# Optimization experiments

Measured on AMD Instinct MI355X. Metric: run time of the kernel, lower is better.

## Reference

```python
import jax, jax.numpy as jnp
import numpy as np

INPUT_SIZE = 1024
OUTPUT_SIZE = 1024
B, S = 4, 2048


def setup_inputs() -> dict:
    key = jax.random.key(0)
    k1, k2, k3, k4, k5, k6 = jax.random.split(key, 6)
    scale = 1.0 / np.sqrt(INPUT_SIZE)
    return {
        "inputs_for_keys": jax.random.normal(k1, (B, S, INPUT_SIZE), jnp.float32),
        "inputs_for_values": jax.random.normal(k2, (B, S, INPUT_SIZE), jnp.float32),
        "inputs_for_queries": jax.random.normal(k3, (B, S, INPUT_SIZE), jnp.float32),
        "W_k": jax.random.normal(k4, (INPUT_SIZE, OUTPUT_SIZE), jnp.float32) * scale,
        "W_v": jax.random.normal(k5, (INPUT_SIZE, OUTPUT_SIZE), jnp.float32) * scale,
        "W_q": jax.random.normal(k6, (INPUT_SIZE, OUTPUT_SIZE), jnp.float32) * scale,
    }


def reference(inputs_for_keys, inputs_for_values, inputs_for_queries, W_k, W_v, W_q):
    # Linear projections (bias=False): x @ W  -> [B, S, D_out]
    K = jnp.einsum("bsi,io->bso", inputs_for_keys, W_k)
    V = jnp.einsum("bsi,io->bso", inputs_for_values, W_v)
    Q = jnp.einsum("bqi,io->bqo", inputs_for_queries, W_q)
    d_k = K.shape[-1]
    # scores: [B, Sq, Sk], scaled by sqrt(embedding_size of K)
    scores = jnp.einsum("bqd,bkd->bqk", Q, K) / jnp.sqrt(jnp.asarray(d_k, Q.dtype))
    # causal mask: positions k > q masked to -inf (use_mask=True since is_self_attention)
    q_idx = jnp.arange(Q.shape[1])[:, None]
    k_idx = jnp.arange(K.shape[1])[None, :]
    scores = jnp.where(k_idx > q_idx, jnp.asarray(-jnp.inf, scores.dtype), scores)
    weights = jax.nn.softmax(scores, axis=-1)
    # output: [B, Sq, D_out]
    return jnp.einsum("bqk,bkd->bqd", weights, V)
```

## Files before the change

### kernel.cpp

```cpp
#include <hip/hip_runtime.h>


typedef __attribute__((ext_vector_type(8))) short short8;
typedef __attribute__((ext_vector_type(4))) float floatx4;

static constexpr long long XE = 8388608LL;
static constexpr long long WE = 1048576LL;

static __device__ __forceinline__ unsigned short f2b(float f) {
  unsigned u = __builtin_bit_cast(unsigned, f);
  u = (u + 0x7fffu + ((u >> 16) & 1u)) >> 16;
  return (unsigned short)u;
}

static __device__ __forceinline__ void gload16(const unsigned short* g, unsigned short* l) {
  __builtin_amdgcn_global_load_lds(
      (const __attribute__((address_space(1))) unsigned int*)g,
      (__attribute__((address_space(3))) unsigned int*)l, 16, 0, 0);
}

#define VMCNT(n) asm volatile("s_waitcnt vmcnt(" #n ")" ::: "memory")
#define LGKM0() asm volatile("s_waitcnt lgkmcnt(0)" ::: "memory")
#define BARRIER() do { asm volatile("" ::: "memory"); __builtin_amdgcn_s_barrier(); asm volatile("" ::: "memory"); } while (0)

#define STAGE(base, matoff, h, slot, kt) do {                                  \
    const unsigned short* _s = (base) + (h) * 131072 + (kt) * 64;              \
    char* _d = sb + (slot) * 65536 + (matoff) + (h) * 16384 + dwave;           \
    gload16(_s, (unsigned short*)_d);                                          \
    gload16(_s + 65536, (unsigned short*)(_d + 8192));                         \
  } while (0)

#define READ_A(slot, mb) do {                                                  \
    const char* _p = sb + (slot) * 65536 + aoffb + (mb) * 2048;                \
    af[0][0] = *(const short8*)(_p + c0);        af[0][1] = *(const short8*)(_p + c1); \
    af[1][0] = *(const short8*)(_p + 2048 + c0); af[1][1] = *(const short8*)(_p + 2048 + c1); \
    af[2][0] = *(const short8*)(_p + 4096 + c0); af[2][1] = *(const short8*)(_p + 4096 + c1); \
    af[3][0] = *(const short8*)(_p + 6144 + c0); af[3][1] = *(const short8*)(_p + 6144 + c1); \
  } while (0)

#define READ_B(slot, nb, bfx) do {                                             \
    const char* _p = sb + (slot) * 65536 + boffb + (nb) * 2048;                \
    bfx[0][0] = *(const short8*)(_p + c0);        bfx[0][1] = *(const short8*)(_p + c1); \
    bfx[1][0] = *(const short8*)(_p + 2048 + c0); bfx[1][1] = *(const short8*)(_p + 2048 + c1); \
  } while (0)

#define MF16(MB, NB, bfx) do {                                                 \
    __builtin_amdgcn_s_setprio(1);                                             \
    _Pragma("unroll")                                                          \
    for (int _m = 0; _m < 4; ++_m) {                                           \
      _Pragma("unroll")                                                        \
      for (int _n = 0; _n < 2; ++_n) {                                         \
        acc[(MB) + _m][(NB) + _n] = __builtin_amdgcn_mfma_f32_16x16x32_bf16(   \
            af[_m][0], bfx[_n][0], acc[(MB) + _m][(NB) + _n], 0, 0, 0);        \
        acc[(MB) + _m][(NB) + _n] = __builtin_amdgcn_mfma_f32_16x16x32_bf16(   \
            af[_m][1], bfx[_n][1], acc[(MB) + _m][(NB) + _n], 0, 0, 0);        \
      } }                                                                      \
    __builtin_amdgcn_s_setprio(0);                                             \
  } while (0)

#define KLOOP8()                                                               \
  STAGE(Ab, 0, 0, 0, 0);     STAGE(Ab, 0, 1, 0, 0);                            \
  STAGE(Bb, 32768, 0, 0, 0); STAGE(Bb, 32768, 1, 0, 0);                        \
  STAGE(Bb, 32768, 0, 1, 1); STAGE(Bb, 32768, 1, 1, 1);                        \
  VMCNT(4);                                                                    \
  BARRIER();                                                                   \
  for (int t = 0; t < 8; ++t) {                                                \
    const int kt1 = 2 * t + 1, kt2 = 2 * t + 2, kt3 = 2 * t + 3;               \
    const bool pf = t < 7;                                                     \
    READ_A(0, 0); READ_B(0, 0, bf0);                                           \
    STAGE(Ab, 0, 0, 1, kt1);                                                   \
    BARRIER(); LGKM0();                                                        \
    MF16(0, 0, bf0);                                                           \
    BARRIER();                                                                 \
    READ_B(0, 2, bf1);                                                         \
    STAGE(Ab, 0, 1, 1, kt1);                                                   \
    BARRIER(); LGKM0();                                                        \
    MF16(0, 2, bf1);                                                           \
    BARRIER();                                                                 \
    READ_A(0, 4);                                                              \
    if (pf) STAGE(Bb, 32768, 0, 0, kt2);                                       \
    BARRIER(); LGKM0();                                                        \
    MF16(4, 2, bf1);                                                           \
    BARRIER();                                                                 \
    if (pf) STAGE(Bb, 32768, 1, 0, kt2);                                       \
    BARRIER();                                                                 \
    MF16(4, 0, bf0);                                                           \
    if (pf) { VMCNT(4); } else { VMCNT(0); }                                   \
    BARRIER();                                                                 \
    READ_A(1, 0); READ_B(1, 0, bf0);                                           \
    if (pf) STAGE(Ab, 0, 0, 0, kt2);                                           \
    BARRIER(); LGKM0();                                                        \
    MF16(0, 0, bf0);                                                           \
    BARRIER();                                                                 \
    READ_B(1, 2, bf1);                                                         \
    if (pf) STAGE(Ab, 0, 1, 0, kt2);                                           \
    BARRIER(); LGKM0();                                                        \
    MF16(0, 2, bf1);                                                           \
    BARRIER();                                                                 \
    READ_A(1, 4);                                                              \
    if (pf) STAGE(Bb, 32768, 0, 1, kt3);                                       \
    BARRIER(); LGKM0();                                                        \
    MF16(4, 2, bf1);                                                           \
    BARRIER();                                                                 \
    if (pf) STAGE(Bb, 32768, 1, 1, kt3);                                       \
    BARRIER();                                                                 \
    MF16(4, 0, bf0);                                                           \
    if (pf) { VMCNT(4); } else { VMCNT(0); }                                   \
    BARRIER();                                                                 \
  }

__global__ __launch_bounds__(512, 2) void projTV8(
    const unsigned short* __restrict__ Xb, const unsigned short* __restrict__ WvT,
    const unsigned short* __restrict__ Gt, unsigned short* __restrict__ Tb,
    unsigned short* __restrict__ Vt) {
  extern __shared__ char sb[];
  const int orig = blockIdx.x;
  const int w = (orig & 7) * 32 + (orig >> 3);
  const unsigned short *Aop, *Bop;
  unsigned short* C;
  int ldc, bi, bj;
  if (w < 128) { Aop = Xb + XE; Bop = Gt; C = Tb; ldc = 1024; bi = w >> 2; bj = w & 3; }
  else { const int j = w - 128; Aop = WvT; Bop = Xb; C = Vt; ldc = 8192; bi = j & 3; bj = j >> 2; }

  const int tid = threadIdx.x, wave = tid >> 6, lane = tid & 63;
  const int wm = wave >> 2, wn = wave & 3, frow = lane & 15, hi = lane >> 4;
  const int r0 = tid >> 3, p0 = ((tid & 7) ^ (r0 & 7)) * 8;
  const int dwave = wave * 1024;
  const int sx = frow & 7;
  const int c0 = (hi ^ sx) * 16, c1 = ((4 + hi) ^ sx) * 16;
  const int aoffb = (wm * 128 + frow) * 128;
  const int boffb = 32768 + (wn * 64 + frow) * 128;
  const unsigned short* Ab = Aop + (long long)(bi * 256 + r0) * 1024 + p0;
  const unsigned short* Bb = Bop + (long long)(bj * 256 + r0) * 1024 + p0;

  short8 af[4][2], bf0[2][2], bf1[2][2];
  floatx4 acc[8][4] = {};

  KLOOP8();

  const long long crow0 = (long long)bi * 256 + wm * 128 + hi * 4;
  const int ccol = bj * 256 + wn * 64 + frow;
#pragma unroll
  for (int m = 0; m < 8; ++m)
#pragma unroll
    for (int j = 0; j < 4; ++j) {
      unsigned short* cp = C + (crow0 + m * 16 + j) * (long long)ldc + ccol;
#pragma unroll
      for (int n = 0; n < 4; ++n) cp[n * 16] = f2b(acc[m][n][j]);
    }
}

__global__ __launch_bounds__(512, 2) void scores_exp8(
    const unsigned short* __restrict__ Tb, const unsigned short* __restrict__ Xk,
    unsigned short* __restrict__ P, float* __restrict__ Rpart) {
  extern __shared__ char sb[];
  const int orig = blockIdx.x;
  const int w = (orig & 7) * 18 + (orig >> 3);
  const int b = w / 36;
  int t2 = w - b * 36;
  int bi = 0;
  while (t2 >= bi + 1) { t2 -= bi + 1; ++bi; }
  const int bj = t2;

  const unsigned short* Aop = Tb + (long long)b * 2048 * 1024;
  const unsigned short* Bop = Xk + (long long)b * 2048 * 1024;

  const int tid = threadIdx.x, wave = tid >> 6, lane = tid & 63;
  const int wm = wave >> 2, wn = wave & 3, frow = lane & 15, hi = lane >> 4;
  const int r0 = tid >> 3, p0 = ((tid & 7) ^ (r0 & 7)) * 8;
  const int dwave = wave * 1024;
  const int sx = frow & 7;
  const int c0 = (hi ^ sx) * 16, c1 = ((4 + hi) ^ sx) * 16;
  const int aoffb = (wm * 128 + frow) * 128;
  const int boffb = 32768 + (wn * 64 + frow) * 128;
  const unsigned short* Ab = Aop + (long long)(bi * 256 + r0) * 1024 + p0;
  const unsigned short* Bb = Bop + (long long)(bj * 256 + r0) * 1024 + p0;

  short8 af[4][2], bf0[2][2], bf1[2][2];
  floatx4 acc[8][4] = {};

  KLOOP8();

  const bool diag = (bi == bj);
  unsigned short* C = P + (long long)b * 2048 * 2048;
  float rs[8][4];
#pragma unroll
  for (int m = 0; m < 8; ++m)
#pragma unroll
    for (int j = 0; j < 4; ++j) {
      const int row_loc = wm * 128 + hi * 4 + m * 16 + j;
      const int row_glob = bi * 256 + row_loc;
      unsigned short* cp = C + (long long)row_glob * 2048 + bj * 256 + wn * 64 + frow;
      float s = 0.f;
#pragma unroll
      for (int n = 0; n < 4; ++n) {
        const int col = bj * 256 + wn * 64 + n * 16 + frow;
        float e = __expf(acc[m][n][j] * 0.03125f);
        if (diag && col > row_glob) e = 0.f;
        cp[n * 16] = f2b(e);
        s += e;
      }
      s += __shfl_xor(s, 1);
      s += __shfl_xor(s, 2);
      s += __shfl_xor(s, 4);
      s += __shfl_xor(s, 8);
      rs[m][j] = s;
    }
  __syncthreads();
  float* red = (float*)sb;
  if (frow == 0) {
#pragma unroll
    for (int m = 0; m < 8; ++m)
#pragma unroll
      for (int j = 0; j < 4; ++j)
        red[(wm * 128 + hi * 4 + m * 16 + j) * 4 + wn] = rs[m][j];
  }
  __syncthreads();
  if (tid < 256)
    Rpart[((long long)b * 8 + bj) * 2048 + bi * 256 + tid] =
        red[tid * 4] + red[tid * 4 + 1] + red[tid * 4 + 2] + red[tid * 4 + 3];
}

template <int NF>
static __device__ __forceinline__ void gemm_loop(
    const unsigned short* __restrict__ A, const unsigned short* __restrict__ Bt,
    int lda, int ldb, int nk, int bi, int bj,
    unsigned short* lA, unsigned short* lB, floatx4 acc[4][NF]) {
  const int t = threadIdx.x, wave = t >> 6, lane = t & 63;
  const int wr = wave >> 1, wc = wave & 1;
  const int sr = lane >> 3;
  const int sc = ((lane & 7) ^ sr) * 8;
  const unsigned short* gA = A + (long long)(bi * 128 + wave * 32 + sr) * lda + sc;
  const unsigned short* gB = Bt + (long long)(bj * (NF * 32) + wave * (NF * 8) + sr) * ldb + sc;
  unsigned short* lAw = lA + wave * 2048;
  unsigned short* lBw = lB + wave * (NF * 512);
  const int frow = lane & 15, hi = lane >> 4;

  for (int ks = 0; ks < nk; ++ks) {
    const long long k0 = (long long)ks * 64;
    __syncthreads();
#pragma unroll
    for (int g = 0; g < 4; ++g)
      gload16(gA + (long long)g * 8 * lda + k0, lAw + g * 512);
#pragma unroll
    for (int g = 0; g < NF; ++g)
      gload16(gB + (long long)g * 8 * ldb + k0, lBw + g * 512);
    __syncthreads();
#pragma unroll
    for (int kk = 0; kk < 2; ++kk) {
      const int ch = (kk * 4 + hi) ^ (frow & 7);
      short8 af[4], bf[NF];
#pragma unroll
      for (int m = 0; m < 4; ++m)
        af[m] = *(const short8*)&lA[(wr * 64 + m * 16 + frow) * 64 + ch * 8];
#pragma unroll
      for (int n = 0; n < NF; ++n)
        bf[n] = *(const short8*)&lB[(wc * (NF * 16) + n * 16 + frow) * 64 + ch * 8];
#pragma unroll
      for (int m = 0; m < 4; ++m)
#pragma unroll
        for (int n = 0; n < NF; ++n)
          acc[m][n] = __builtin_amdgcn_mfma_f32_16x16x32_bf16(af[m], bf[n], acc[m][n], 0, 0, 0);
    }
  }
}

__global__ __launch_bounds__(256) void gt_kernel(
    const unsigned short* __restrict__ WkB, const unsigned short* __restrict__ WqB,
    unsigned short* __restrict__ Gt) {
  __shared__ __align__(16) unsigned short lA[8192], lB[8192];
  floatx4 acc[4][4] = {};
  gemm_loop<4>(WkB, WqB, 1024, 1024, 16, blockIdx.x, blockIdx.y, lA, lB, acc);
  const int tid = threadIdx.x, wave = tid >> 6, lane = tid & 63;
  const int wr = wave >> 1, wc = wave & 1, frow = lane & 15, hi = lane >> 4;
  const long long crow0 = (long long)blockIdx.x * 128 + wr * 64 + hi * 4;
  const int ccol = blockIdx.y * 128 + wc * 64 + frow;
#pragma unroll
  for (int m = 0; m < 4; ++m)
#pragma unroll
    for (int j = 0; j < 4; ++j) {
      unsigned short* cp = Gt + (crow0 + m * 16 + j) * 1024 + ccol;
#pragma unroll
      for (int n = 0; n < 4; ++n) cp[n * 16] = f2b(acc[m][n][j]);
    }
}

__global__ __launch_bounds__(256) void rowsum(
    const float* __restrict__ Rpart, float* __restrict__ Rinv) {
  const int t = blockIdx.x * 256 + threadIdx.x;
  const int b = t >> 11, row = t & 2047;
  const int nb = (row >> 8) + 1;
  float s = 0.f;
  for (int bj = 0; bj < nb; ++bj) s += Rpart[(b * 8 + bj) * 2048 + row];
  Rinv[t] = 1.f / s;
}

__global__ __launch_bounds__(256) void pv_kernel(
    const unsigned short* __restrict__ P, const unsigned short* __restrict__ Vt,
    const float* __restrict__ Rinv, float* __restrict__ out) {
  __shared__ __align__(16) unsigned short lA[8192], lB[4096];
  const int orig = blockIdx.x;
  const int c = orig & 7, i = orig >> 3;
  const int bi = 15 - (i >> 3);
  const int rr = (i & 7) + c * 8;
  const int b = rr >> 4, bj = rr & 15;
  floatx4 acc[4][2] = {};
  gemm_loop<2>(P + (long long)b * 2048 * 2048, Vt + (long long)b * 2048, 2048, 8192,
               (bi + 1) * 2, bi, bj, lA, lB, acc);
  const int tid = threadIdx.x, wave = tid >> 6, lane = tid & 63;
  const int wr = wave >> 1, wc = wave & 1, frow = lane & 15, hi = lane >> 4;
  float* C = out + (long long)b * 2048 * 1024;
  const float* Ri = Rinv + b * 2048;
#pragma unroll
  for (int m = 0; m < 4; ++m)
#pragma unroll
    for (int j = 0; j < 4; ++j) {
      const int row = bi * 128 + wr * 64 + hi * 4 + m * 16 + j;
      const float riv = Ri[row];
      float* cp = C + (long long)row * 1024 + bj * 64 + wc * 32 + frow;
      cp[0] = acc[m][0][j] * riv;
      cp[16] = acc[m][1][j] * riv;
    }
}

__global__ __launch_bounds__(256) void cvtAll(
    const float* __restrict__ Xk, const float* __restrict__ Xv,
    const float* __restrict__ Xq, const float* __restrict__ Wq,
    const float* __restrict__ Wk, const float* __restrict__ Wv,
    unsigned short* __restrict__ Xb, unsigned short* __restrict__ WqB,
    unsigned short* __restrict__ WkB, unsigned short* __restrict__ WvT) {
  __shared__ unsigned short tile[64][65];
  const int bx = blockIdx.x, t = threadIdx.x;
  if (bx < 1536) {
    const int y = bx / 512, sub = bx - y * 512;
    const float* in = y == 0 ? Xv : (y == 1 ? Xq : Xk);
    unsigned short* o = Xb + (long long)y * XE;
    const int n8 = (int)(XE / 8), stride = 512 * 256;
    for (int i = sub * 256 + t; i < n8; i += stride) {
      float4 a = ((const float4*)in)[2 * i];
      float4 d = ((const float4*)in)[2 * i + 1];
      short8 v;
      v[0] = (short)f2b(a.x); v[1] = (short)f2b(a.y);
      v[2] = (short)f2b(a.z); v[3] = (short)f2b(a.w);
      v[4] = (short)f2b(d.x); v[5] = (short)f2b(d.y);
      v[6] = (short)f2b(d.z); v[7] = (short)f2b(d.w);
      ((short8*)o)[i] = v;
    }
  } else if (bx < 1792) {
    const int w2 = bx - 1536;
    const int y = w2 >> 7, sub = w2 & 127;
    const float* in = y == 0 ? Wq : Wk;
    unsigned short* o = y == 0 ? WqB : WkB;
    const int n8 = (int)(WE / 8), stride = 128 * 256;
    for (int i = sub * 256 + t; i < n8; i += stride) {
      float4 a = ((const float4*)in)[2 * i];
      float4 d = ((const float4*)in)[2 * i + 1];
      short8 v;
      v[0] = (short)f2b(a.x); v[1] = (short)f2b(a.y);
      v[2] = (short)f2b(a.z); v[3] = (short)f2b(a.w);
      v[4] = (short)f2b(d.x); v[5] = (short)f2b(d.y);
      v[6] = (short)f2b(d.z); v[7] = (short)f2b(d.w);
      ((short8*)o)[i] = v;
    }
  } else {
    const int v = bx - 1792;
    const int i0 = (v & 15) * 64, j0 = (v >> 4) * 64;
#pragma unroll
    for (int r = 0; r < 16; ++r) {
      int lin = r * 256 + t;
      int i = lin >> 6, j = lin & 63;
      tile[i][j] = f2b(Wv[(long long)(i0 + i) * 1024 + j0 + j]);
    }
    __syncthreads();
#pragma unroll
    for (int r = 0; r < 16; ++r) {
      int lin = r * 256 + t;
      int o = lin >> 6, i = lin & 63;
      WvT[(long long)(j0 + o) * 1024 + i0 + i] = tile[i][o];
    }
  }
}

extern "C" void kernel_launch(void* const* d_in, const int* in_sizes, int n_in,
                              void* d_out, int out_size, void* d_ws, size_t ws_size,
                              hipStream_t stream) {
  const float* Xk = (const float*)d_in[0];
  const float* Xv = (const float*)d_in[1];
  const float* Xq = (const float*)d_in[2];
  const float* Wk = (const float*)d_in[3];
  const float* Wv = (const float*)d_in[4];
  const float* Wq = (const float*)d_in[5];
  float* out = (float*)d_out;

  unsigned short* ws = (unsigned short*)d_ws;
  unsigned short* Xb = ws;
  unsigned short* WqB = ws + 3 * XE;
  unsigned short* WkB = WqB + WE;
  unsigned short* WvT = WkB + WE;
  unsigned short* Gt = WvT + WE;
  unsigned short* Tb = Gt + WE;
  unsigned short* Vt = Tb + XE;
  float* Rpart = (float*)(Vt + XE);
  float* Rinv = Rpart + 4 * 8 * 2048;
  unsigned short* Pbuf = ws;

  cvtAll<<<2048, 256, 0, stream>>>(Xk, Xv, Xq, Wq, Wk, Wv, Xb, WqB, WkB, WvT);
  gt_kernel<<<dim3(8, 8), 256, 0, stream>>>(WkB, WqB, Gt);
  projTV8<<<256, 512, 131072, stream>>>(Xb, WvT, Gt, Tb, Vt);
  scores_exp8<<<144, 512, 131072, stream>>>(Tb, Xb + 2 * XE, Pbuf, Rpart);
  rowsum<<<32, 256, 0, stream>>>(Rpart, Rinv);
  pv_kernel<<<1024, 256, 0, stream>>>(Pbuf, Vt, Rinv, out);
}
```

Before: 150.1 us.

## Fuse Xq fp32-to-bf16 conversion into projection GEMM A-operand loading

The Xq conversion pass is dropped from cvtAll. The T-projection GEMM now loads fp32 Xq directly into registers, converts it to bf16 and writes it into LDS inside the pipelined K loop, while the B operand still uses async global-to-LDS loads. This removes a 32MB fp32 read plus a 16MB bf16 write-and-reread round trip. In exchange the fp32 register staging adds register pressure, and launch bounds drop from 2 to 1 blocks per CU, which may reduce occupancy and latency hiding for both branches of the kernel.

```diff
diff --git a/kernel.cpp b/kernel.cpp
--- a/kernel.cpp
+++ b/kernel.cpp
@@ -109,19 +109,90 @@
     BARRIER();                                                                 \
   }
 
-__global__ __launch_bounds__(512, 2) void projTV8(
-    const unsigned short* __restrict__ Xb, const unsigned short* __restrict__ WvT,
-    const unsigned short* __restrict__ Gt, unsigned short* __restrict__ Tb,
-    unsigned short* __restrict__ Vt) {
+#define FLOAD(st, h, kt) do {                                                  \
+    const float* _s = Fq + (h) * 131072 + (kt) * 64;                           \
+    fr[st][0] = *(const floatx4*)_s;                                           \
+    fr[st][1] = *(const floatx4*)(_s + 4);                                     \
+    fr[st][2] = *(const floatx4*)(_s + 65536);                                 \
+    fr[st][3] = *(const floatx4*)(_s + 65540);                                 \
+  } while (0)
+
+#define FWRITE(st, h, slot) do {                                               \
+    char* _d = sb + (slot) * 65536 + (h) * 16384 + dwave + lane * 16;          \
+    short8 _v0, _v1;                                                           \
+    _Pragma("unroll")                                                          \
+    for (int _e = 0; _e < 4; ++_e) {                                           \
+      _v0[_e]     = (short)f2b(fr[st][0][_e]);                                 \
+      _v0[_e + 4] = (short)f2b(fr[st][1][_e]);                                 \
+      _v1[_e]     = (short)f2b(fr[st][2][_e]);                                 \
+      _v1[_e + 4] = (short)f2b(fr[st][3][_e]);                                 \
+    }                                                                          \
+    *(short8*)_d = _v0;                                                        \
+    *(short8*)(_d + 8192) = _v1;                                               \
+  } while (0)
+
+#define KLOOP8F()                                                              \
+  FLOAD(0, 0, 0); FLOAD(1, 1, 0);                                              \
+  STAGE(Bb, 32768, 0, 0, 0); STAGE(Bb, 32768, 1, 0, 0);                        \
+  STAGE(Bb, 32768, 0, 1, 1); STAGE(Bb, 32768, 1, 1, 1);                        \
+  FWRITE(0, 0, 0); FWRITE(1, 1, 0);                                            \
+  VMCNT(4); LGKM0();                                                           \
+  BARRIER();                                                                   \
+  for (int t = 0; t < 8; ++t) {                                                \
+    const int kt1 = 2 * t + 1, kt2 = 2 * t + 2, kt3 = 2 * t + 3;               \
+    const bool pf = t < 7;                                                     \
+    READ_A(0, 0); READ_B(0, 0, bf0);                                           \
+    FLOAD(0, 0, kt1);                                                          \
+    BARRIER(); LGKM0();                                                        \
+    MF16(0, 0, bf0);                                                           \
+    BARRIER();                                                                 \
+    READ_B(0, 2, bf1);                                                         \
+    FLOAD(1, 1, kt1);                                                          \
+    BARRIER(); LGKM0();                                                        \
+    MF16(0, 2, bf1);                                                           \
+    BARRIER();                                                                 \
+    READ_A(0, 4);                                                              \
+    if (pf) STAGE(Bb, 32768, 0, 0, kt2);                                       \
+    BARRIER(); LGKM0();                                                        \
+    MF16(4, 2, bf1);                                                           \
+    BARRIER();                                                                 \
+    if (pf) STAGE(Bb, 32768, 1, 0, kt2);                                       \
+    BARRIER();                                                                 \
+    MF16(4, 0, bf0);                                                           \
+    FWRITE(0, 0, 1); FWRITE(1, 1, 1);                                          \
+    if (pf) { VMCNT(4); } else { VMCNT(0); }                                   \
+    LGKM0();                                                                   \
+    BARRIER();                                                                 \
+    READ_A(1, 0); READ_B(1, 0, bf0);                                           \
+    if (pf) FLOAD(0, 0, kt2);                                                  \
+    BARRIER(); LGKM0();                                                        \
+    MF16(0, 0, bf0);                                                           \
+    BARRIER();                                                                 \
+    READ_B(1, 2, bf1);                                                         \
+    if (pf) FLOAD(1, 1, kt2);                                                  \
+    BARRIER(); LGKM0();                                                        \
+    MF16(0, 2, bf1);                                                           \
+    BARRIER();                                                                 \
+    READ_A(1, 4);                                                              \
+    if (pf) STAGE(Bb, 32768, 0, 1, kt3);                                       \
+    BARRIER(); LGKM0();                                                        \
+    MF16(4, 2, bf1);                                                           \
+    BARRIER();                                                                 \
+    if (pf) STAGE(Bb, 32768, 1, 1, kt3);                                       \
+    BARRIER();                                                                 \
+    MF16(4, 0, bf0);                                                           \
+    if (pf) { FWRITE(0, 0, 0); FWRITE(1, 1, 0); VMCNT(4); LGKM0(); }           \
+    else { VMCNT(0); }                                                         \
+    BARRIER();                                                                 \
+  }
+
+__global__ __launch_bounds__(512, 1) void projTV8(
+    const float* __restrict__ XqF, const unsigned short* __restrict__ Xb,
+    const unsigned short* __restrict__ WvT, const unsigned short* __restrict__ Gt,
+    unsigned short* __restrict__ Tb, unsigned short* __restrict__ Vt) {
   extern __shared__ char sb[];
   const int orig = blockIdx.x;
   const int w = (orig & 7) * 32 + (orig >> 3);
-  const unsigned short *Aop, *Bop;
-  unsigned short* C;
-  int ldc, bi, bj;
-  if (w < 128) { Aop = Xb + XE; Bop = Gt; C = Tb; ldc = 1024; bi = w >> 2; bj = w & 3; }
-  else { const int j = w - 128; Aop = WvT; Bop = Xb; C = Vt; ldc = 8192; bi = j & 3; bj = j >> 2; }
-
   const int tid = threadIdx.x, wave = tid >> 6, lane = tid & 63;
   const int wm = wave >> 2, wn = wave & 3, frow = lane & 15, hi = lane >> 4;
   const int r0 = tid >> 3, p0 = ((tid & 7) ^ (r0 & 7)) * 8;
@@ -130,13 +201,25 @@
   const int c0 = (hi ^ sx) * 16, c1 = ((4 + hi) ^ sx) * 16;
   const int aoffb = (wm * 128 + frow) * 128;
   const int boffb = 32768 + (wn * 64 + frow) * 128;
-  const unsigned short* Ab = Aop + (long long)(bi * 256 + r0) * 1024 + p0;
-  const unsigned short* Bb = Bop + (long long)(bj * 256 + r0) * 1024 + p0;
 
   short8 af[4][2], bf0[2][2], bf1[2][2];
+  floatx4 fr[2][4];
   floatx4 acc[8][4] = {};
-
-  KLOOP8();
+  unsigned short* C;
+  int ldc, bi, bj;
+
+  if (w < 128) {
+    bi = w >> 2; bj = w & 3; C = Tb; ldc = 1024;
+    const float* Fq = XqF + (long long)(bi * 256 + r0) * 1024 + p0;
+    const unsigned short* Bb = Gt + (long long)(bj * 256 + r0) * 1024 + p0;
+    KLOOP8F();
+  } else {
+    const int j = w - 128;
+    bi = j & 3; bj = j >> 2; C = Vt; ldc = 8192;
+    const unsigned short* Ab = WvT + (long long)(bi * 256 + r0) * 1024 + p0;
+    const unsigned short* Bb = Xb + (long long)(bj * 256 + r0) * 1024 + p0;
+    KLOOP8();
+  }
 
   const long long crow0 = (long long)bi * 256 + wm * 128 + hi * 4;
   const int ccol = bj * 256 + wn * 64 + frow;
@@ -325,16 +408,16 @@
 
 __global__ __launch_bounds__(256) void cvtAll(
     const float* __restrict__ Xk, const float* __restrict__ Xv,
-    const float* __restrict__ Xq, const float* __restrict__ Wq,
-    const float* __restrict__ Wk, const float* __restrict__ Wv,
-    unsigned short* __restrict__ Xb, unsigned short* __restrict__ WqB,
-    unsigned short* __restrict__ WkB, unsigned short* __restrict__ WvT) {
+    const float* __restrict__ Wq, const float* __restrict__ Wk,
+    const float* __restrict__ Wv, unsigned short* __restrict__ Xb,
+    unsigned short* __restrict__ WqB, unsigned short* __restrict__ WkB,
+    unsigned short* __restrict__ WvT) {
   __shared__ unsigned short tile[64][65];
   const int bx = blockIdx.x, t = threadIdx.x;
-  if (bx < 1536) {
-    const int y = bx / 512, sub = bx - y * 512;
-    const float* in = y == 0 ? Xv : (y == 1 ? Xq : Xk);
-    unsigned short* o = Xb + (long long)y * XE;
+  if (bx < 1024) {
+    const int y = bx >> 9, sub = bx & 511;
+    const float* in = y == 0 ? Xv : Xk;
+    unsigned short* o = Xb + (y == 0 ? 0 : 2 * XE);
     const int n8 = (int)(XE / 8), stride = 512 * 256;
     for (int i = sub * 256 + t; i < n8; i += stride) {
       float4 a = ((const float4*)in)[2 * i];
@@ -346,8 +429,8 @@
       v[6] = (short)f2b(d.z); v[7] = (short)f2b(d.w);
       ((short8*)o)[i] = v;
     }
-  } else if (bx < 1792) {
-    const int w2 = bx - 1536;
+  } else if (bx < 1280) {
+    const int w2 = bx - 1024;
     const int y = w2 >> 7, sub = w2 & 127;
     const float* in = y == 0 ? Wq : Wk;
     unsigned short* o = y == 0 ? WqB : WkB;
@@ -363,7 +446,7 @@
       ((short8*)o)[i] = v;
     }
   } else {
-    const int v = bx - 1792;
+    const int v = bx - 1280;
     const int i0 = (v & 15) * 64, j0 = (v >> 4) * 64;
 #pragma unroll
     for (int r = 0; r < 16; ++r) {
@@ -404,9 +487,9 @@
   float* Rinv = Rpart + 4 * 8 * 2048;
   unsigned short* Pbuf = ws;
 
-  cvtAll<<<2048, 256, 0, stream>>>(Xk, Xv, Xq, Wq, Wk, Wv, Xb, WqB, WkB, WvT);
+  cvtAll<<<1536, 256, 0, stream>>>(Xk, Xv, Wq, Wk, Wv, Xb, WqB, WkB, WvT);
   gt_kernel<<<dim3(8, 8), 256, 0, stream>>>(WkB, WqB, Gt);
-  projTV8<<<256, 512, 131072, stream>>>(Xb, WvT, Gt, Tb, Vt);
+  projTV8<<<256, 512, 131072, stream>>>(Xq, Xb, WvT, Gt, Tb, Vt);
   scores_exp8<<<144, 512, 131072, stream>>>(Tb, Xb + 2 * XE, Pbuf, Rpart);
   rowsum<<<32, 256, 0, stream>>>(Rpart, Rinv);
   pv_kernel<<<1024, 256, 0, stream>>>(Pbuf, Vt, Rinv, out);
```

Result: slower. 159.6 us (+6.3%).
